# Kernel tuning notes

Measured on AMD Instinct MI355X. Metric: run time of the kernel, lower is better.

## Reference

```python
import jax, jax.numpy as jnp
import numpy as np

D = 768
H = 16
DK = D // H
DFF = 3072
POOL = 100
NCLS = 7
EPS = 1e-6


def layer_norm(x, a, b):
    # torch: (x - mean) / (std + eps), std unbiased (ddof=1)
    mean = jnp.mean(x, axis=-1, keepdims=True)
    var = jnp.sum((x - mean) ** 2, axis=-1, keepdims=True) / (x.shape[-1] - 1)
    return a * (x - mean) / (jnp.sqrt(var) + EPS) + b


def mha(x, Wq, bq, Wk, bk, Wv, bv, Wo, bo):
    B, S, _ = x.shape
    def split(h):
        return h.reshape(B, S, H, DK).transpose(0, 2, 1, 3)  # [B,H,S,DK]
    q = split(x @ Wq + bq)
    k = split(x @ Wk + bk)
    v = split(x @ Wv + bv)
    scores = jnp.einsum('bhqd,bhkd->bhqk', q, k) / jnp.sqrt(jnp.float32(DK))
    p = jax.nn.softmax(scores, axis=-1)
    o = jnp.einsum('bhqk,bhkd->bhqd', p, v)
    o = o.transpose(0, 2, 1, 3).reshape(B, S, D)
    return o @ Wo + bo


def setup_inputs() -> dict:
    key = jax.random.key(0)
    ks = jax.random.split(key, 24)
    B, S = 8, 1023
    s = 0.02
    inp = {
        'text_features': jax.random.normal(ks[0], (B, S, D), jnp.float32),
        'prompt_pool': jax.random.normal(ks[1], (POOL, D), jnp.float32),
        'cls_token': jax.random.normal(ks[2], (1, 1, D), jnp.float32),
        'Wq': jax.random.normal(ks[3], (D, D), jnp.float32) * s,
        'bq': jnp.zeros((D,), jnp.float32),
        'Wk': jax.random.normal(ks[4], (D, D), jnp.float32) * s,
        'bk': jnp.zeros((D,), jnp.float32),
        'Wv': jax.random.normal(ks[5], (D, D), jnp.float32) * s,
        'bv': jnp.zeros((D,), jnp.float32),
        'Wo': jax.random.normal(ks[6], (D, D), jnp.float32) * s,
        'bo': jnp.zeros((D,), jnp.float32),
        'ln1_a': jnp.ones((D,), jnp.float32),
        'ln1_b': jnp.zeros((D,), jnp.float32),
        'ln2_a': jnp.ones((D,), jnp.float32),
        'ln2_b': jnp.zeros((D,), jnp.float32),
        'W1': jax.random.normal(ks[7], (D, DFF), jnp.float32) * s,
        'b1': jnp.zeros((DFF,), jnp.float32),
        'W2': jax.random.normal(ks[8], (DFF, D), jnp.float32) * s,
        'b2': jnp.zeros((D,), jnp.float32),
        'lnf_a': jnp.ones((D,), jnp.float32),
        'lnf_b': jnp.zeros((D,), jnp.float32),
        'Wpool': jax.random.normal(ks[9], (D, POOL), jnp.float32) * s,
        'bpool': jnp.zeros((POOL,), jnp.float32),
        'Wcls': jax.random.normal(ks[10], (D, NCLS), jnp.float32) * s,
        'bcls': jnp.zeros((NCLS,), jnp.float32),
    }
    return inp


def reference(text_features, prompt_pool, cls_token, Wq, bq, Wk, bk, Wv, bv, Wo, bo,
              ln1_a, ln1_b, ln2_a, ln2_b, W1, b1, W2, b2, lnf_a, lnf_b,
              Wpool, bpool, Wcls, bcls):
    B = text_features.shape[0]
    x = jnp.concatenate([jnp.broadcast_to(cls_token, (B, 1, D)), text_features], axis=1)
    # EncoderLayer (N=1), dropout in eval mode (identity)
    x = x + mha(layer_norm(x, ln1_a, ln1_b), Wq, bq, Wk, bk, Wv, bv, Wo, bo)
    h = layer_norm(x, ln2_a, ln2_b)
    x = x + (jax.nn.relu(h @ W1 + b1) @ W2 + b2)
    x = layer_norm(x, lnf_a, lnf_b)
    cls = x[:, 0, :]  # [B, D]
    probabilities = jax.nn.softmax(cls @ Wpool + bpool, axis=1)  # [B, POOL]
    class_logits = cls @ Wcls + bcls  # [B, NCLS]
    class_probs = jax.nn.softmax(class_logits, axis=1)
    entropy = -jnp.sum(class_probs * jnp.log(class_probs + 1e-9), axis=1)
    max_entropy = jnp.log(jnp.float32(7.0))
    norm_ent = entropy / max_entropy
    adjusted_k = jnp.clip(jnp.floor(1.0 + norm_ent * (POOL - 1)).astype(jnp.int32), 1, POOL)  # [B]
    # full descending top-k (jit-friendly: pad to POOL instead of data-dependent max_k)
    _, top_idx = jax.lax.top_k(probabilities, POOL)  # [B, POOL]
    gathered = prompt_pool[top_idx]  # [B, POOL, D]
    keep = (jnp.arange(POOL)[None, :] < adjusted_k[:, None]).astype(prompt_pool.dtype)
    selected_prompts = gathered * keep[:, :, None]
    return (selected_prompts, class_logits)
```

## Files before the change

kernel.cpp:

```cpp
#include <hip/hip_runtime.h>


#define OUT_CLS_OFF 614400

__device__ __forceinline__ float bsum256(float v, float* red) {
    int lane = threadIdx.x & 63, w = threadIdx.x >> 6;
#pragma unroll
    for (int off = 1; off < 64; off <<= 1) v += __shfl_xor(v, off);
    __syncthreads();
    if (lane == 0) red[w] = v;
    __syncthreads();
    return red[0] + red[1] + red[2] + red[3];
}

__global__ __launch_bounds__(256) void prep_a(
    const float* __restrict__ clsT, const float* __restrict__ ga,
    const float* __restrict__ gb, const float* __restrict__ Wq,
    const float* __restrict__ bq, const float* __restrict__ Wk,
    float* __restrict__ q0, float* __restrict__ colw, int* __restrict__ cnts)
{
    __shared__ float ys[768];
    __shared__ float red[4];
    __shared__ float4 partA[16][17];
    __shared__ float4 partB[16][17];
    int t = threadIdx.x;
    if (blockIdx.x == 0 && t < 16) cnts[t] = 0;
    if (blockIdx.x < 12) {
        float a0 = clsT[t], a1 = clsT[t + 256], a2 = clsT[t + 512];
        float mean = bsum256(a0 + a1 + a2, red) * (1.0f / 768.0f);
        float d0 = a0 - mean, d1 = a1 - mean, d2 = a2 - mean;
        float var = bsum256(d0 * d0 + d1 * d1 + d2 * d2, red) * (1.0f / 767.0f);
        float den = sqrtf(var) + 1e-6f;
        ys[t]       = (ga[t] * d0) / den + gb[t];
        ys[t + 256] = (ga[t + 256] * d1) / den + gb[t + 256];
        ys[t + 512] = (ga[t + 512] * d2) / den + gb[t + 512];
        __syncthreads();
        int c = blockIdx.x * 64 + (t & 15) * 4;
        int kq = t >> 4;
        float4 acc = {0.f, 0.f, 0.f, 0.f};
#pragma unroll 8
        for (int i = 0; i < 48; ++i) {
            int k = kq * 48 + i;
            float4 w = *(const float4*)&Wq[(size_t)k * 768 + c];
            float y = ys[k];
            acc.x = fmaf(y, w.x, acc.x); acc.y = fmaf(y, w.y, acc.y);
            acc.z = fmaf(y, w.z, acc.z); acc.w = fmaf(y, w.w, acc.w);
        }
        partA[kq][t & 15] = acc;
        __syncthreads();
        if (t < 16) {
            float4 s = {0.f, 0.f, 0.f, 0.f};
#pragma unroll
            for (int i = 0; i < 16; ++i) {
                float4 v = partA[i][t];
                s.x += v.x; s.y += v.y; s.z += v.z; s.w += v.w;
            }
            int cc = blockIdx.x * 64 + t * 4;
            float4 b4 = *(const float4*)&bq[cc];
            q0[cc] = s.x + b4.x; q0[cc + 1] = s.y + b4.y;
            q0[cc + 2] = s.z + b4.z; q0[cc + 3] = s.w + b4.w;
        }
    } else {
        int c = (blockIdx.x - 12) * 64 + (t & 15) * 4;
        int kq = t >> 4;
        float4 aa = {0.f, 0.f, 0.f, 0.f}, ab = {0.f, 0.f, 0.f, 0.f};
#pragma unroll 8
        for (int i = 0; i < 48; ++i) {
            int k = kq * 48 + i;
            float4 w = *(const float4*)&Wk[(size_t)k * 768 + c];
            float g = ga[k], h = gb[k];
            aa.x = fmaf(g, w.x, aa.x); aa.y = fmaf(g, w.y, aa.y);
            aa.z = fmaf(g, w.z, aa.z); aa.w = fmaf(g, w.w, aa.w);
            ab.x = fmaf(h, w.x, ab.x); ab.y = fmaf(h, w.y, ab.y);
            ab.z = fmaf(h, w.z, ab.z); ab.w = fmaf(h, w.w, ab.w);
        }
        partA[kq][t & 15] = aa;
        partB[kq][t & 15] = ab;
        __syncthreads();
        if (t < 16) {
            float4 sa = {0.f, 0.f, 0.f, 0.f}, sb = {0.f, 0.f, 0.f, 0.f};
#pragma unroll
            for (int i = 0; i < 16; ++i) {
                float4 va = partA[i][t], vb = partB[i][t];
                sa.x += va.x; sa.y += va.y; sa.z += va.z; sa.w += va.w;
                sb.x += vb.x; sb.y += vb.y; sb.z += vb.z; sb.w += vb.w;
            }
            int cc = (blockIdx.x - 12) * 64 + t * 4;
            *(float4*)&colw[cc] = sa;
            *(float4*)&colw[768 + cc] = sb;
        }
    }
}

__global__ __launch_bounds__(256) void prep_b(
    const float* __restrict__ Wk, const float* __restrict__ bk,
    const float* __restrict__ q0, const float* __restrict__ colw,
    float* __restrict__ wkqc)
{
    __shared__ float qs[768];
    int t = threadIdx.x;
    qs[t] = q0[t]; qs[t + 256] = q0[t + 256]; qs[t + 512] = q0[t + 512];
    __syncthreads();
    const float invs = 0.14433756729740643f;
    int kl = t >> 4, h = t & 15;
    int k = blockIdx.x * 16 + kl;
    const float* wr = Wk + (size_t)k * 768 + h * 48;
    const float* qh = qs + h * 48;
    float a = 0.f;
#pragma unroll
    for (int d = 0; d < 48; d += 4) {
        float4 w = *(const float4*)&wr[d];
        a += w.x * qh[d] + w.y * qh[d + 1] + w.z * qh[d + 2] + w.w * qh[d + 3];
    }
    wkqc[k * 16 + h] = a * invs;
    if (blockIdx.x == 0 && t < 16) {
        float cd = 0.f, sa = 0.f, sb = 0.f;
        for (int d = 0; d < 48; ++d) {
            int dd = t * 48 + d;
            cd = fmaf(bk[dd], qs[dd], cd);
            sa = fmaf(colw[dd], qs[dd], sa);
            sb = fmaf(colw[768 + dd], qs[dd], sb);
        }
        wkqc[12304 + t] = sa * invs;
        wkqc[12320 + t] = sb * invs + cd * invs;
    }
}

__global__ __launch_bounds__(256) void ln_scores(
    const float* __restrict__ tf, const float* __restrict__ clsT,
    const float* __restrict__ ga, const float* __restrict__ wkqc,
    float* __restrict__ sc, float2* __restrict__ stats)
{
    __shared__ float tr[256][17];
    __shared__ float partw[4][16];
    __shared__ float red[2][4][2];
    int t = threadIdx.x;
    int l = t & 63, w = t >> 6;

    float wk0[16], wk1[16], wk2[16];
    {
        const float4* p0 = (const float4*)(wkqc + t * 16);
        const float4* p1 = (const float4*)(wkqc + (t + 256) * 16);
        const float4* p2 = (const float4*)(wkqc + (t + 512) * 16);
#pragma unroll
        for (int q = 0; q < 4; ++q) {
            float4 v0 = p0[q], v1 = p1[q], v2 = p2[q];
            wk0[q * 4] = v0.x; wk0[q * 4 + 1] = v0.y; wk0[q * 4 + 2] = v0.z; wk0[q * 4 + 3] = v0.w;
            wk1[q * 4] = v1.x; wk1[q * 4 + 1] = v1.y; wk1[q * 4 + 2] = v1.z; wk1[q * 4 + 3] = v1.w;
            wk2[q * 4] = v2.x; wk2[q * 4 + 1] = v2.y; wk2[q * 4 + 2] = v2.z; wk2[q * 4 + 3] = v2.w;
        }
    }
    float ga0 = ga[t], ga1 = ga[t + 256], ga2 = ga[t + 512];
    float Sg = wkqc[12304 + (t & 15)];
    float Cg = wkqc[12320 + (t & 15)];

    int r0 = blockIdx.x * 8;
    int b = r0 >> 10, j0 = r0 & 1023;
    const float* src0 = j0 ? (tf + ((size_t)b * 1023 + (j0 - 1)) * 768) : clsT;
    float x0 = src0[t], x1 = src0[t + 256], x2 = src0[t + 512];
    for (int r = 0; r < 8; ++r) {
        int j = j0 + r;
        float cx0 = x0, cx1 = x1, cx2 = x2;
        if (r < 7) {
            const float* sp = tf + ((size_t)b * 1023 + j) * 768;
            x0 = sp[t]; x1 = sp[t + 256]; x2 = sp[t + 512];
        }
        float s1 = cx0 + cx1 + cx2;
        float s2 = fmaf(cx0, cx0, fmaf(cx1, cx1, cx2 * cx2));
        float g0 = ga0 * cx0, g1 = ga1 * cx1, g2 = ga2 * cx2;
        float dt[16];
#pragma unroll
        for (int h = 0; h < 16; ++h)
            dt[h] = fmaf(g0, wk0[h], fmaf(g1, wk1[h], g2 * wk2[h]));
#pragma unroll
        for (int off = 1; off < 64; off <<= 1) {
            s1 += __shfl_xor(s1, off);
            s2 += __shfl_xor(s2, off);
        }
        if (l == 0) { red[r & 1][w][0] = s1; red[r & 1][w][1] = s2; }
#pragma unroll
        for (int h = 0; h < 16; ++h) tr[t][h] = dt[h];
        __syncthreads();
        int hh = t & 15, ch = t >> 4;
        float v = 0.f;
#pragma unroll
        for (int i = 0; i < 16; ++i) v += tr[ch * 16 + i][hh];
        v += __shfl_xor(v, 16);
        v += __shfl_xor(v, 32);
        if (l < 16) partw[w][l] = v;
        __syncthreads();
        if (t < 16) {
            float dtot = partw[0][t] + partw[1][t] + partw[2][t] + partw[3][t];
            float s1t = red[r & 1][0][0] + red[r & 1][1][0] + red[r & 1][2][0] + red[r & 1][3][0];
            float s2t = red[r & 1][0][1] + red[r & 1][1][1] + red[r & 1][2][1] + red[r & 1][3][1];
            float mean = s1t * (1.0f / 768.0f);
            float var = (s2t - mean * s1t) * (1.0f / 767.0f);
            float rden = 1.0f / (sqrtf(var) + 1e-6f);
            float sv = rden * (dtot - mean * Sg) + Cg;
            sc[(((size_t)b * 16 + t) << 10) + j] = expf(sv) * rden;
            if (t == 0) stats[(b << 10) + j] = make_float2(mean, rden);
        }
    }
}

__global__ __launch_bounds__(256) void upart_k(
    const float* __restrict__ tf, const float* __restrict__ clsT,
    const float* __restrict__ sc, const float2* __restrict__ stats,
    float* __restrict__ up, float* __restrict__ upz, float* __restrict__ upc1)
{
    __shared__ float qs_s[16][32];
    __shared__ float2 sst[32];
    int b = blockIdx.x & 7, jc = blockIdx.x >> 3;
    int t = threadIdx.x;
    if (t < 128) {
        int h = t >> 3, j4 = (t & 7) * 4;
        float4 pv = *(const float4*)(sc + (((size_t)b * 16 + h) << 10) + jc * 32 + j4);
        qs_s[h][j4] = pv.x; qs_s[h][j4 + 1] = pv.y;
        qs_s[h][j4 + 2] = pv.z; qs_s[h][j4 + 3] = pv.w;
    } else if (t < 160) {
        sst[t - 128] = stats[(b << 10) + jc * 32 + (t - 128)];
    }
    __syncthreads();
    float acc[16][3];
#pragma unroll
    for (int h = 0; h < 16; ++h) { acc[h][0] = 0.f; acc[h][1] = 0.f; acc[h][2] = 0.f; }
    int j0 = jc * 32;
    const float* sp0 = j0 ? (tf + ((size_t)b * 1023 + (j0 - 1)) * 768) : clsT;
    float nx0 = sp0[t], nx1 = sp0[t + 256], nx2 = sp0[t + 512];
    for (int jj = 0; jj < 32; ++jj) {
        float x0 = nx0, x1 = nx1, x2 = nx2;
        if (jj < 31) {
            const float* sp = tf + ((size_t)b * 1023 + j0 + jj) * 768;
            nx0 = sp[t]; nx1 = sp[t + 256]; nx2 = sp[t + 512];
        }
#pragma unroll
        for (int h = 0; h < 16; ++h) {
            float qh = qs_s[h][jj];
            acc[h][0] = fmaf(qh, x0, acc[h][0]);
            acc[h][1] = fmaf(qh, x1, acc[h][1]);
            acc[h][2] = fmaf(qh, x2, acc[h][2]);
        }
    }
    float* o = up + (((size_t)b * 32 + jc) * 16) * 768;
#pragma unroll
    for (int h = 0; h < 16; ++h) {
        o[h * 768 + t] = acc[h][0];
        o[h * 768 + t + 256] = acc[h][1];
        o[h * 768 + t + 512] = acc[h][2];
    }
    if (t < 16) {
        float zp = 0.f, cp = 0.f;
        for (int jj = 0; jj < 32; ++jj) {
            float wv = qs_s[t][jj];
            float2 st = sst[jj];
            zp += wv / st.y;
            cp += wv * st.x;
        }
        upz[((size_t)b * 32 + jc) * 16 + t] = zp;
        upc1[((size_t)b * 32 + jc) * 16 + t] = cp;
    }
}

__global__ __launch_bounds__(256) void o0_k(
    const float* __restrict__ up, const float* __restrict__ upz,
    const float* __restrict__ upc1, const float* __restrict__ ga,
    const float* __restrict__ gb, const float* __restrict__ Wv,
    const float* __restrict__ bv, float* __restrict__ o0)
{
    __shared__ float us[768];
    __shared__ float part[4][64];
    int h = blockIdx.x, b = blockIdx.y, t = threadIdx.x;
    float s0 = 0.f, s1 = 0.f, s2 = 0.f;
#pragma unroll 8
    for (int jc = 0; jc < 32; ++jc) {
        const float* q = up + (((size_t)b * 32 + jc) * 16 + h) * 768;
        s0 += q[t]; s1 += q[t + 256]; s2 += q[t + 512];
    }
    float Z = 0.f, c1r = 0.f;
#pragma unroll 8
    for (int jc = 0; jc < 32; ++jc) {
        Z   += upz[((size_t)b * 32 + jc) * 16 + h];
        c1r += upc1[((size_t)b * 32 + jc) * 16 + h];
    }
    float rz = 1.0f / Z;
    us[t]       = ga[t] * ((s0 - c1r) * rz) + gb[t];
    us[t + 256] = ga[t + 256] * ((s1 - c1r) * rz) + gb[t + 256];
    us[t + 512] = ga[t + 512] * ((s2 - c1r) * rz) + gb[t + 512];
    __syncthreads();
    int dd = t & 63, kg = t >> 6;
    float a = 0.f;
    if (dd < 48) {
#pragma unroll 8
        for (int i = 0; i < 192; ++i) {
            int k = kg * 192 + i;
            a = fmaf(us[k], Wv[(size_t)k * 768 + h * 48 + dd], a);
        }
    }
    part[kg][dd] = a;
    __syncthreads();
    if (t < 48)
        o0[(size_t)b * 768 + h * 48 + t] =
            part[0][t] + part[1][t] + part[2][t] + part[3][t] + bv[h * 48 + t];
}

__global__ __launch_bounds__(256) void x2_k(
    const float* __restrict__ o0, const float* __restrict__ Wo,
    const float* __restrict__ bo, const float* __restrict__ clsT,
    float* __restrict__ x2w)
{
    __shared__ float ys[768];
    __shared__ float4 part[16][17];
    int b = blockIdx.y, t = threadIdx.x;
    const float* xr = o0 + (size_t)b * 768;
    ys[t] = xr[t]; ys[t + 256] = xr[t + 256]; ys[t + 512] = xr[t + 512];
    __syncthreads();
    int c = blockIdx.x * 64 + (t & 15) * 4;
    int kq = t >> 4;
    float4 acc = {0.f, 0.f, 0.f, 0.f};
#pragma unroll 8
    for (int i = 0; i < 48; ++i) {
        int k = kq * 48 + i;
        float4 w = *(const float4*)&Wo[(size_t)k * 768 + c];
        float y = ys[k];
        acc.x = fmaf(y, w.x, acc.x); acc.y = fmaf(y, w.y, acc.y);
        acc.z = fmaf(y, w.z, acc.z); acc.w = fmaf(y, w.w, acc.w);
    }
    part[kq][t & 15] = acc;
    __syncthreads();
    if (t < 16) {
        float4 s = {0.f, 0.f, 0.f, 0.f};
#pragma unroll
        for (int i = 0; i < 16; ++i) {
            float4 v = part[i][t];
            s.x += v.x; s.y += v.y; s.z += v.z; s.w += v.w;
        }
        int cc = blockIdx.x * 64 + t * 4;
        float4 b4 = *(const float4*)&bo[cc];
        float4 r4 = *(const float4*)&clsT[cc];
        float* o = x2w + (size_t)b * 768 + cc;
        o[0] = s.x + b4.x + r4.x; o[1] = s.y + b4.y + r4.y;
        o[2] = s.z + b4.z + r4.z; o[3] = s.w + b4.w + r4.w;
    }
}

__global__ __launch_bounds__(256) void f1_k(
    const float* __restrict__ x2w, const float* __restrict__ ga,
    const float* __restrict__ gb, const float* __restrict__ W1,
    const float* __restrict__ b1, float* __restrict__ f1w)
{
    __shared__ float ys[768];
    __shared__ float red[4];
    __shared__ float4 part[8][33];
    int b = blockIdx.y, t = threadIdx.x;
    const float* xr = x2w + (size_t)b * 768;
    float a0 = xr[t], a1 = xr[t + 256], a2 = xr[t + 512];
    float mean = bsum256(a0 + a1 + a2, red) * (1.0f / 768.0f);
    float d0 = a0 - mean, d1 = a1 - mean, d2 = a2 - mean;
    float var = bsum256(d0 * d0 + d1 * d1 + d2 * d2, red) * (1.0f / 767.0f);
    float den = sqrtf(var) + 1e-6f;
    ys[t]       = (ga[t] * d0) / den + gb[t];
    ys[t + 256] = (ga[t + 256] * d1) / den + gb[t + 256];
    ys[t + 512] = (ga[t + 512] * d2) / den + gb[t + 512];
    __syncthreads();
    int c = blockIdx.x * 128 + (t & 31) * 4;
    int kq = t >> 5;
    float4 acc = {0.f, 0.f, 0.f, 0.f};
#pragma unroll 8
    for (int i = 0; i < 96; ++i) {
        int k = kq * 96 + i;
        float4 w = *(const float4*)&W1[(size_t)k * 3072 + c];
        float y = ys[k];
        acc.x = fmaf(y, w.x, acc.x); acc.y = fmaf(y, w.y, acc.y);
        acc.z = fmaf(y, w.z, acc.z); acc.w = fmaf(y, w.w, acc.w);
    }
    part[kq][t & 31] = acc;
    __syncthreads();
    if (t < 32) {
        float4 s = {0.f, 0.f, 0.f, 0.f};
#pragma unroll
        for (int i = 0; i < 8; ++i) {
            float4 v = part[i][t];
            s.x += v.x; s.y += v.y; s.z += v.z; s.w += v.w;
        }
        int cc = blockIdx.x * 128 + t * 4;
        float4 b4 = *(const float4*)&b1[cc];
        float* o = f1w + (size_t)b * 3072 + cc;
        o[0] = fmaxf(s.x + b4.x, 0.f); o[1] = fmaxf(s.y + b4.y, 0.f);
        o[2] = fmaxf(s.z + b4.z, 0.f); o[3] = fmaxf(s.w + b4.w, 0.f);
    }
}

__global__ __launch_bounds__(256) void x3_k(
    const float* __restrict__ f1w, const float* __restrict__ W2,
    const float* __restrict__ b2, const float* __restrict__ x2w,
    float* __restrict__ x3w)
{
    __shared__ float ys[3072];
    __shared__ float4 part[16][17];
    int b = blockIdx.y, t = threadIdx.x;
    const float* xr = f1w + (size_t)b * 3072;
    for (int i = t; i < 3072; i += 256) ys[i] = xr[i];
    __syncthreads();
    int c = blockIdx.x * 64 + (t & 15) * 4;
    int kq = t >> 4;
    float4 acc = {0.f, 0.f, 0.f, 0.f};
#pragma unroll 8
    for (int i = 0; i < 192; ++i) {
        int k = kq * 192 + i;
        float4 w = *(const float4*)&W2[(size_t)k * 768 + c];
        float y = ys[k];
        acc.x = fmaf(y, w.x, acc.x); acc.y = fmaf(y, w.y, acc.y);
        acc.z = fmaf(y, w.z, acc.z); acc.w = fmaf(y, w.w, acc.w);
    }
    part[kq][t & 15] = acc;
    __syncthreads();
    if (t < 16) {
        float4 s = {0.f, 0.f, 0.f, 0.f};
#pragma unroll
        for (int i = 0; i < 16; ++i) {
            float4 v = part[i][t];
            s.x += v.x; s.y += v.y; s.z += v.z; s.w += v.w;
        }
        int cc = blockIdx.x * 64 + t * 4;
        float4 b4 = *(const float4*)&b2[cc];
        const float* x2r = x2w + (size_t)b * 768 + cc;
        float* o = x3w + (size_t)b * 768 + cc;
        o[0] = x2r[0] + s.x + b4.x; o[1] = x2r[1] + s.y + b4.y;
        o[2] = x2r[2] + s.z + b4.z; o[3] = x2r[3] + s.w + b4.w;
    }
}

__global__ __launch_bounds__(256) void logits_part(
    const float* __restrict__ x3w, const float* __restrict__ ga,
    const float* __restrict__ gb, const float* __restrict__ Wpool,
    const float* __restrict__ Wcls, double* __restrict__ lp,
    const float* __restrict__ bpool, const float* __restrict__ bcls,
    float* __restrict__ out, int* __restrict__ topw, int* __restrict__ kkw,
    int* __restrict__ cnts)
{
    __shared__ float ys[768];
    __shared__ float red[4];
    __shared__ double sPd[100];
    __shared__ double sC7d[7];
    __shared__ int sOld;
    int kg = blockIdx.x, b = blockIdx.y, t = threadIdx.x;
    const float* xr = x3w + (size_t)b * 768;
    float a0 = xr[t], a1 = xr[t + 256], a2 = xr[t + 512];
    float mean = bsum256(a0 + a1 + a2, red) * (1.0f / 768.0f);
    float d0 = a0 - mean, d1 = a1 - mean, d2 = a2 - mean;
    float var = bsum256(d0 * d0 + d1 * d1 + d2 * d2, red) * (1.0f / 767.0f);
    float den = sqrtf(var) + 1e-6f;
    ys[t]       = (ga[t] * d0) / den + gb[t];
    ys[t + 256] = (ga[t + 256] * d1) / den + gb[t + 256];
    ys[t + 512] = (ga[t + 512] * d2) / den + gb[t + 512];
    __syncthreads();
    int kbase = kg * 96;
    if (t < 100) {
        double a = 0.0;
#pragma unroll 8
        for (int i = 0; i < 96; ++i) {
            int k = kbase + i;
            a = fma((double)ys[k], (double)Wpool[k * 100 + t], a);
        }
        lp[((size_t)b * 8 + kg) * 112 + t] = a;
    } else if (t < 107) {
        int c = t - 100;
        double a = 0.0;
#pragma unroll 8
        for (int i = 0; i < 96; ++i) {
            int k = kbase + i;
            a = fma((double)ys[k], (double)Wcls[k * 7 + c], a);
        }
        lp[((size_t)b * 8 + kg) * 112 + t] = a;
    }

    __syncthreads();
    __threadfence();
    if (t == 0)
        sOld = __hip_atomic_fetch_add(&cnts[b], 1, __ATOMIC_ACQ_REL,
                                      __HIP_MEMORY_SCOPE_AGENT);
    __syncthreads();
    if (sOld != 7) return;

    if (t < 107) {
        double a = (t < 100) ? (double)bpool[t] : (double)bcls[t - 100];
#pragma unroll
        for (int g = 0; g < 8; ++g) a += lp[((size_t)b * 8 + g) * 112 + t];
        if (t < 100) sPd[t] = a;
        else {
            sC7d[t - 100] = a;
            out[OUT_CLS_OFF + b * 7 + (t - 100)] = (float)a;
        }
    }
    __syncthreads();
    if (t == 0) {
        double m7 = sC7d[0];
        for (int j = 1; j < 7; ++j) m7 = fmax(m7, sC7d[j]);
        double es[7]; double z = 0.0;
        for (int j = 0; j < 7; ++j) { es[j] = exp(sC7d[j] - m7); z += es[j]; }
        double ent = 0.0;
        for (int j = 0; j < 7; ++j) { double pr = es[j] / z; ent -= pr * log(pr + 1e-9); }
        double ne = ent / log(7.0);
        int kk = (int)floor(1.0 + ne * 99.0);
        kkw[b] = kk < 1 ? 1 : (kk > 100 ? 100 : kk);
    }
    if (t < 100) {
        double pi = sPd[t];
        int r = 0;
#pragma unroll 4
        for (int j = 0; j < 100; ++j) {
            double pj = sPd[j];
            r += (pj > pi) || (pj == pi && j < t);
        }
        topw[b * 100 + r] = t;
    }
}

__global__ __launch_bounds__(192) void gather_k(
    const float* __restrict__ pool, const int* __restrict__ topw,
    const int* __restrict__ kkw, float* __restrict__ out)
{
    int r = blockIdx.x, b = blockIdx.y, t = threadIdx.x;
    int idx = topw[b * 100 + r];
    bool keep = r < kkw[b];
    const float4* src = (const float4*)(pool + (size_t)idx * 768);
    float4* dst = (float4*)(out + (size_t)b * 76800 + (size_t)r * 768);
    float4 z = {0.f, 0.f, 0.f, 0.f};
    dst[t] = keep ? src[t] : z;
}

extern "C" void kernel_launch(void* const* d_in, const int* in_sizes, int n_in,
                              void* d_out, int out_size, void* d_ws, size_t ws_size,
                              hipStream_t stream) {
    (void)in_sizes; (void)n_in; (void)out_size; (void)ws_size;
    const float* tf    = (const float*)d_in[0];
    const float* pool  = (const float*)d_in[1];
    const float* clsT  = (const float*)d_in[2];
    const float* Wq    = (const float*)d_in[3];
    const float* bq    = (const float*)d_in[4];
    const float* Wk    = (const float*)d_in[5];
    const float* bk    = (const float*)d_in[6];
    const float* Wv    = (const float*)d_in[7];
    const float* bv    = (const float*)d_in[8];
    const float* Wo    = (const float*)d_in[9];
    const float* bo    = (const float*)d_in[10];
    const float* ln1a  = (const float*)d_in[11];
    const float* ln1b  = (const float*)d_in[12];
    const float* ln2a  = (const float*)d_in[13];
    const float* ln2b  = (const float*)d_in[14];
    const float* W1    = (const float*)d_in[15];
    const float* b1    = (const float*)d_in[16];
    const float* W2    = (const float*)d_in[17];
    const float* b2    = (const float*)d_in[18];
    const float* lnfa  = (const float*)d_in[19];
    const float* lnfb  = (const float*)d_in[20];
    const float* Wpool = (const float*)d_in[21];
    const float* bpool = (const float*)d_in[22];
    const float* Wcls  = (const float*)d_in[23];
    const float* bcls  = (const float*)d_in[24];
    float* out = (float*)d_out;
    char* ws = (char*)d_ws;

    float*  sc    = (float*)(ws + 0);
    float2* stats = (float2*)(ws + 524288);
    float*  wkqc  = (float*)(ws + 589824);
    float*  q0    = (float*)(ws + 639232);
    float*  colw  = (float*)(ws + 642304);
    float*  up    = (float*)(ws + 648448);
    float*  upz   = (float*)(ws + 13231360);
    float*  upc1  = (float*)(ws + 13247744);
    float*  o0    = (float*)(ws + 13264128);
    float*  x2w   = (float*)(ws + 13288704);
    float*  f1w   = (float*)(ws + 13313280);
    float*  x3w   = (float*)(ws + 13411584);
    int*    topw  = (int*)(ws + 13436160);
    int*    kkw   = (int*)(ws + 13439360);
    double* lp    = (double*)(ws + 13439392);
    int*    cnts  = (int*)(ws + 13496736);

    prep_a<<<24, 256, 0, stream>>>(clsT, ln1a, ln1b, Wq, bq, Wk, q0, colw, cnts);
    prep_b<<<48, 256, 0, stream>>>(Wk, bk, q0, colw, wkqc);
    ln_scores<<<1024, 256, 0, stream>>>(tf, clsT, ln1a, wkqc, sc, stats);
    upart_k<<<256, 256, 0, stream>>>(tf, clsT, sc, stats, up, upz, upc1);
    o0_k<<<dim3(16, 8), 256, 0, stream>>>(up, upz, upc1, ln1a, ln1b, Wv, bv, o0);
    x2_k<<<dim3(12, 8), 256, 0, stream>>>(o0, Wo, bo, clsT, x2w);
    f1_k<<<dim3(24, 8), 256, 0, stream>>>(x2w, ln2a, ln2b, W1, b1, f1w);
    x3_k<<<dim3(12, 8), 256, 0, stream>>>(f1w, W2, b2, x2w, x3w);
    logits_part<<<dim3(8, 8), 256, 0, stream>>>(x3w, lnfa, lnfb, Wpool, Wcls,
                                                lp, bpool, bcls, out, topw,
                                                kkw, cnts);
    gather_k<<<dim3(100, 8), 192, 0, stream>>>(pool, topw, kkw, out);
}
```

Baseline: 108.5 us.

## Fuse score computation and value partial-sum kernels into one pass

Merges ln_scores and upart_k into a single kernel, so each block computes the per-row LayerNorm stats and attention weights for 32 rows and immediately accumulates the weighted text features. This removes the intermediate score and stats buffers and a second read of text_features from global memory. The cost is fewer blocks (256 instead of 1024), more serial work per block with an extra barrier per row, and higher register pressure from the 48 accumulators plus the held weights.

```diff
diff --git a/kernel.cpp b/kernel.cpp
--- a/kernel.cpp
+++ b/kernel.cpp
@@ -126,14 +126,15 @@
     }
 }
 
-__global__ __launch_bounds__(256) void ln_scores(
+__global__ __launch_bounds__(256) void score_upart(
     const float* __restrict__ tf, const float* __restrict__ clsT,
     const float* __restrict__ ga, const float* __restrict__ wkqc,
-    float* __restrict__ sc, float2* __restrict__ stats)
+    float* __restrict__ up, float* __restrict__ upz, float* __restrict__ upc1)
 {
     __shared__ float tr[256][17];
     __shared__ float partw[4][16];
     __shared__ float red[2][4][2];
+    __shared__ float wrow[16];
     int t = threadIdx.x;
     int l = t & 63, w = t >> 6;
 
@@ -154,40 +155,50 @@
     float Sg = wkqc[12304 + (t & 15)];
     float Cg = wkqc[12320 + (t & 15)];
 
-    int r0 = blockIdx.x * 8;
-    int b = r0 >> 10, j0 = r0 & 1023;
+    float acc0[16], acc1[16], acc2[16];
+#pragma unroll
+    for (int h = 0; h < 16; ++h) { acc0[h] = 0.f; acc1[h] = 0.f; acc2[h] = 0.f; }
+    float zacc = 0.f, c1acc = 0.f;
+
+    int b = blockIdx.x & 7, jc = blockIdx.x >> 3;
+    int j0 = jc * 32;
     const float* src0 = j0 ? (tf + ((size_t)b * 1023 + (j0 - 1)) * 768) : clsT;
     float x0 = src0[t], x1 = src0[t + 256], x2 = src0[t + 512];
-    for (int r = 0; r < 8; ++r) {
+
+    for (int r = 0; r < 32; ++r) {
         int j = j0 + r;
         float cx0 = x0, cx1 = x1, cx2 = x2;
-        if (r < 7) {
+        if (r < 31) {
             const float* sp = tf + ((size_t)b * 1023 + j) * 768;
             x0 = sp[t]; x1 = sp[t + 256]; x2 = sp[t + 512];
         }
         float s1 = cx0 + cx1 + cx2;
         float s2 = fmaf(cx0, cx0, fmaf(cx1, cx1, cx2 * cx2));
         float g0 = ga0 * cx0, g1 = ga1 * cx1, g2 = ga2 * cx2;
-        float dt[16];
-#pragma unroll
-        for (int h = 0; h < 16; ++h)
-            dt[h] = fmaf(g0, wk0[h], fmaf(g1, wk1[h], g2 * wk2[h]));
-#pragma unroll
-        for (int off = 1; off < 64; off <<= 1) {
-            s1 += __shfl_xor(s1, off);
-            s2 += __shfl_xor(s2, off);
-        }
-        if (l == 0) { red[r & 1][w][0] = s1; red[r & 1][w][1] = s2; }
-#pragma unroll
-        for (int h = 0; h < 16; ++h) tr[t][h] = dt[h];
+        {
+            float dt[16];
+#pragma unroll
+            for (int h = 0; h < 16; ++h)
+                dt[h] = fmaf(g0, wk0[h], fmaf(g1, wk1[h], g2 * wk2[h]));
+#pragma unroll
+            for (int off = 1; off < 64; off <<= 1) {
+                s1 += __shfl_xor(s1, off);
+                s2 += __shfl_xor(s2, off);
+            }
+            if (l == 0) { red[r & 1][w][0] = s1; red[r & 1][w][1] = s2; }
+#pragma unroll
+            for (int h = 0; h < 16; ++h) tr[t][h] = dt[h];
+        }
         __syncthreads();
-        int hh = t & 15, ch = t >> 4;
-        float v = 0.f;
-#pragma unroll
-        for (int i = 0; i < 16; ++i) v += tr[ch * 16 + i][hh];
-        v += __shfl_xor(v, 16);
-        v += __shfl_xor(v, 32);
-        if (l < 16) partw[w][l] = v;
+        {
+            int hh = t & 15, ch = t >> 4;
+            float v = 0.f;
+#pragma unroll
+            for (int i = 0; i < 16; ++i) v += tr[ch * 16 + i][hh];
+            v += __shfl_xor(v, 16);
+            v += __shfl_xor(v, 32);
+            if (l < 16) partw[w][l] = v;
+        }
         __syncthreads();
         if (t < 16) {
             float dtot = partw[0][t] + partw[1][t] + partw[2][t] + partw[3][t];
@@ -197,67 +208,32 @@
             float var = (s2t - mean * s1t) * (1.0f / 767.0f);
             float rden = 1.0f / (sqrtf(var) + 1e-6f);
             float sv = rden * (dtot - mean * Sg) + Cg;
-            sc[(((size_t)b * 16 + t) << 10) + j] = expf(sv) * rden;
-            if (t == 0) stats[(b << 10) + j] = make_float2(mean, rden);
-        }
-    }
-}
-
-__global__ __launch_bounds__(256) void upart_k(
-    const float* __restrict__ tf, const float* __restrict__ clsT,
-    const float* __restrict__ sc, const float2* __restrict__ stats,
-    float* __restrict__ up, float* __restrict__ upz, float* __restrict__ upc1)
-{
-    __shared__ float qs_s[16][32];
-    __shared__ float2 sst[32];
-    int b = blockIdx.x & 7, jc = blockIdx.x >> 3;
-    int t = threadIdx.x;
-    if (t < 128) {
-        int h = t >> 3, j4 = (t & 7) * 4;
-        float4 pv = *(const float4*)(sc + (((size_t)b * 16 + h) << 10) + jc * 32 + j4);
-        qs_s[h][j4] = pv.x; qs_s[h][j4 + 1] = pv.y;
-        qs_s[h][j4 + 2] = pv.z; qs_s[h][j4 + 3] = pv.w;
-    } else if (t < 160) {
-        sst[t - 128] = stats[(b << 10) + jc * 32 + (t - 128)];
-    }
-    __syncthreads();
-    float acc[16][3];
-#pragma unroll
-    for (int h = 0; h < 16; ++h) { acc[h][0] = 0.f; acc[h][1] = 0.f; acc[h][2] = 0.f; }
-    int j0 = jc * 32;
-    const float* sp0 = j0 ? (tf + ((size_t)b * 1023 + (j0 - 1)) * 768) : clsT;
-    float nx0 = sp0[t], nx1 = sp0[t + 256], nx2 = sp0[t + 512];
-    for (int jj = 0; jj < 32; ++jj) {
-        float x0 = nx0, x1 = nx1, x2 = nx2;
-        if (jj < 31) {
-            const float* sp = tf + ((size_t)b * 1023 + j0 + jj) * 768;
-            nx0 = sp[t]; nx1 = sp[t + 256]; nx2 = sp[t + 512];
-        }
+            float e = expf(sv);
+            float wv = e * rden;
+            wrow[t] = wv;
+            zacc += e;
+            c1acc = fmaf(wv, mean, c1acc);
+        }
+        __syncthreads();
 #pragma unroll
         for (int h = 0; h < 16; ++h) {
-            float qh = qs_s[h][jj];
-            acc[h][0] = fmaf(qh, x0, acc[h][0]);
-            acc[h][1] = fmaf(qh, x1, acc[h][1]);
-            acc[h][2] = fmaf(qh, x2, acc[h][2]);
-        }
-    }
+            float wh = wrow[h];
+            acc0[h] = fmaf(wh, cx0, acc0[h]);
+            acc1[h] = fmaf(wh, cx1, acc1[h]);
+            acc2[h] = fmaf(wh, cx2, acc2[h]);
+        }
+    }
+
     float* o = up + (((size_t)b * 32 + jc) * 16) * 768;
 #pragma unroll
     for (int h = 0; h < 16; ++h) {
-        o[h * 768 + t] = acc[h][0];
-        o[h * 768 + t + 256] = acc[h][1];
-        o[h * 768 + t + 512] = acc[h][2];
+        o[h * 768 + t] = acc0[h];
+        o[h * 768 + t + 256] = acc1[h];
+        o[h * 768 + t + 512] = acc2[h];
     }
     if (t < 16) {
-        float zp = 0.f, cp = 0.f;
-        for (int jj = 0; jj < 32; ++jj) {
-            float wv = qs_s[t][jj];
-            float2 st = sst[jj];
-            zp += wv / st.y;
-            cp += wv * st.x;
-        }
-        upz[((size_t)b * 32 + jc) * 16 + t] = zp;
-        upc1[((size_t)b * 32 + jc) * 16 + t] = cp;
+        upz[((size_t)b * 32 + jc) * 16 + t] = zacc;
+        upc1[((size_t)b * 32 + jc) * 16 + t] = c1acc;
     }
 }
 
@@ -561,27 +537,24 @@
     float* out = (float*)d_out;
     char* ws = (char*)d_ws;
 
-    float*  sc    = (float*)(ws + 0);
-    float2* stats = (float2*)(ws + 524288);
-    float*  wkqc  = (float*)(ws + 589824);
-    float*  q0    = (float*)(ws + 639232);
-    float*  colw  = (float*)(ws + 642304);
-    float*  up    = (float*)(ws + 648448);
-    float*  upz   = (float*)(ws + 13231360);
-    float*  upc1  = (float*)(ws + 13247744);
-    float*  o0    = (float*)(ws + 13264128);
-    float*  x2w   = (float*)(ws + 13288704);
-    float*  f1w   = (float*)(ws + 13313280);
-    float*  x3w   = (float*)(ws + 13411584);
-    int*    topw  = (int*)(ws + 13436160);
-    int*    kkw   = (int*)(ws + 13439360);
-    double* lp    = (double*)(ws + 13439392);
-    int*    cnts  = (int*)(ws + 13496736);
+    float*  wkqc  = (float*)(ws + 0);
+    float*  q0    = (float*)(ws + 49408);
+    float*  colw  = (float*)(ws + 52480);
+    float*  up    = (float*)(ws + 58624);
+    float*  upz   = (float*)(ws + 12641536);
+    float*  upc1  = (float*)(ws + 12657920);
+    float*  o0    = (float*)(ws + 12674304);
+    float*  x2w   = (float*)(ws + 12698880);
+    float*  f1w   = (float*)(ws + 12723456);
+    float*  x3w   = (float*)(ws + 12821760);
+    int*    topw  = (int*)(ws + 12846336);
+    int*    kkw   = (int*)(ws + 12849536);
+    double* lp    = (double*)(ws + 12849568);
+    int*    cnts  = (int*)(ws + 12906912);
 
     prep_a<<<24, 256, 0, stream>>>(clsT, ln1a, ln1b, Wq, bq, Wk, q0, colw, cnts);
     prep_b<<<48, 256, 0, stream>>>(Wk, bk, q0, colw, wkqc);
-    ln_scores<<<1024, 256, 0, stream>>>(tf, clsT, ln1a, wkqc, sc, stats);
-    upart_k<<<256, 256, 0, stream>>>(tf, clsT, sc, stats, up, upz, upc1);
+    score_upart<<<256, 256, 0, stream>>>(tf, clsT, ln1a, wkqc, up, upz, upc1);
     o0_k<<<dim3(16, 8), 256, 0, stream>>>(up, upz, upc1, ln1a, ln1b, Wv, bv, o0);
     x2_k<<<dim3(12, 8), 256, 0, stream>>>(o0, Wo, bo, clsT, x2w);
     f1_k<<<dim3(24, 8), 256, 0, stream>>>(x2w, ln2a, ln2b, W1, b1, f1w);
```

Measured after the change: 115.6 us. +6.6%, slower.
